# Kernel tuning notes

Measured on AMD Instinct MI355X. Metric: run time of the kernel, lower is better.

## Reference

```python
import jax, jax.numpy as jnp
import numpy as np


def setup_inputs() -> dict:
    key = jax.random.key(0)
    k1, k2, k3 = jax.random.split(key, 3)
    B, CIN, T, K = 64, 64, 1, 4096
    COUT, F = 64, 4
    L = F * K  # 16384; gather index space per (b, o)
    x = jax.random.normal(k1, (B, CIN, T, K), dtype=jnp.float32)
    upsample_params = jax.random.normal(k2, (CIN, COUT, F), dtype=jnp.float32)
    indices = jax.random.randint(k3, (L,), 0, L, dtype=jnp.int64 if jax.config.jax_enable_x64 else jnp.int32)
    return {"x": x, "upsample_params": upsample_params, "indices": indices}


def reference(x, upsample_params, indices):
    # x: [B, Cin, T, K]; params: [Cin, Cout, 4] -> res: [B, Cout, 4, K]
    res = jnp.einsum('bitk,iof->bofk', x, upsample_params)
    B, O = res.shape[0], res.shape[1]
    L = indices.shape[0]  # == 4*K
    # torch: flatten + index_select with per-(b,o) offset == gather along last axis
    flat = res.reshape(B, O, L)
    out = jnp.take(flat, indices, axis=2)
    return out.reshape(B, O, 1, L)
```

## Files before the change

kernel.cpp:

```cpp
#include <hip/hip_runtime.h>


typedef __attribute__((ext_vector_type(8))) short short8;
typedef __attribute__((ext_vector_type(4))) float floatx4;

#define NB    64
#define CIN   64
#define COUT  64
#define KDIM  4096
#define LDIM  16384
#define ITERS 8
#define BXS2  72
#define XT_BYTES ((size_t)NB * KDIM * CIN * 2)

__device__ __forceinline__ unsigned short f2bf(float f) {
  union { float f; unsigned u; } v; v.f = f;
  unsigned r = v.u + 0x7FFFu + ((v.u >> 16) & 1u);
  return (unsigned short)(r >> 16);
}

__global__ __launch_bounds__(256) void transpose_bf16(const float* __restrict__ x,
                                                      unsigned short* __restrict__ xt) {
  __shared__ float tile[64 * 65];
  const int t = threadIdx.x;
  const int b = blockIdx.y;
  const int k0 = blockIdx.x * 64;
  const float4* x4 = (const float4*)x;
#pragma unroll
  for (int p = 0; p < 4; ++p) {
    int i  = p * 16 + (t >> 4);
    int kq = t & 15;
    float4 v = x4[(size_t)(b * CIN + i) * (KDIM / 4) + (k0 >> 2) + kq];
    tile[i * 65 + kq * 4 + 0] = v.x;
    tile[i * 65 + kq * 4 + 1] = v.y;
    tile[i * 65 + kq * 4 + 2] = v.z;
    tile[i * 65 + kq * 4 + 3] = v.w;
  }
  __syncthreads();
  unsigned int* xt32 = (unsigned int*)xt;
  const int ip = (t & 31) * 2;
#pragma unroll
  for (int p = 0; p < 8; ++p) {
    int k = p * 8 + (t >> 5);
    unsigned lo = f2bf(tile[ip * 65 + k]);
    unsigned hi = f2bf(tile[(ip + 1) * 65 + k]);
    xt32[((size_t)b * KDIM + k0 + k) * (CIN / 2) + (ip >> 1)] = lo | (hi << 16);
  }
}

__global__ __launch_bounds__(256) void prepack_afrag(const float* __restrict__ p,
                                                     unsigned short* __restrict__ pb) {
  const int t = blockIdx.x * 256 + threadIdx.x;
  const int lane = t & 63;
  const int mk = t >> 6;
  const int mt = mk >> 3, kt = mk & 7;
  const int o = mt * 16 + (lane & 15);
  const int quad = lane >> 4;
#pragma unroll
  for (int j = 0; j < 8; ++j) {
    int s = kt * 32 + quad * 8 + j;
    int i = s & 63, g = s >> 6;
    pb[t * 8 + j] = f2bf(p[(i * COUT + o) * 4 + g]);
  }
}

__global__ __launch_bounds__(256, 4) void gemm_db(const unsigned short* __restrict__ xt,
                                                  const unsigned short* __restrict__ pb,
                                                  const int* __restrict__ idx,
                                                  float* __restrict__ out) {
  __shared__ __align__(16) unsigned short Bx[2][64 * BXS2];
  __shared__ int fpv[2][64];

  const int t = threadIdx.x;
  const int b = blockIdx.y;
  const int w = t >> 6;
  const int lane = t & 63;
  const int lane15 = lane & 15;
  const int quad = lane >> 4;

  short8 af[8];
  {
    const short8* pbv = (const short8*)pb;
#pragma unroll
    for (int kt = 0; kt < 8; ++kt)
      af[kt] = pbv[(w * 8 + kt) * 64 + lane];
  }

  const unsigned short* xb = xt + (size_t)b * KDIM * CIN;
  const int u = t & 3;
  const int lrow = t >> 2;
  const int lb0 = blockIdx.x * (ITERS * 64);

  uint4 d0, d1; int fp, ivn;
  {
    const int iv0 = idx[lb0 + lrow];
    const uint4* r0 = (const uint4*)(xb + (size_t)(iv0 & (KDIM - 1)) * CIN);
    d0 = r0[2 * u];
    d1 = r0[2 * u + 1];
    fp = iv0 >> 12;
    ivn = idx[lb0 + 64 + lrow];
  }

  const short8 z8 = {0, 0, 0, 0, 0, 0, 0, 0};

  for (int it = 0; it < ITERS; ++it) {
    const int p = it & 1;
    *(uint4*)&Bx[p][lrow * BXS2 + u * 16]     = d0;
    *(uint4*)&Bx[p][lrow * BXS2 + u * 16 + 8] = d1;
    if (u == 0) fpv[p][lrow] = fp;
    asm volatile("s_waitcnt lgkmcnt(0)" ::: "memory");
    __builtin_amdgcn_s_barrier();
    asm volatile("" ::: "memory");

    if (it + 1 < ITERS) {
      fp = ivn >> 12;
      const uint4* rn = (const uint4*)(xb + (size_t)(ivn & (KDIM - 1)) * CIN);
      d0 = rn[2 * u];
      d1 = rn[2 * u + 1];
      if (it + 2 < ITERS) ivn = idx[lb0 + (it + 2) * 64 + lrow];
    }

    floatx4 acc[4] = {floatx4{0.f, 0.f, 0.f, 0.f}, floatx4{0.f, 0.f, 0.f, 0.f},
                      floatx4{0.f, 0.f, 0.f, 0.f}, floatx4{0.f, 0.f, 0.f, 0.f}};
#pragma unroll
    for (int nt = 0; nt < 4; ++nt) {
      const int lr = nt * 16 + lane15;
      const short8 ev = *(const short8*)&Bx[p][lr * BXS2 + quad * 8];
      const short8 ov = *(const short8*)&Bx[p][lr * BXS2 + 32 + quad * 8];
      const int fpl = fpv[p][lr];
#pragma unroll
      for (int kt = 0; kt < 8; ++kt) {
        const short8 h  = (kt & 1) ? ov : ev;
        const short8 bf = (fpl == (kt >> 1)) ? h : z8;
        acc[nt] = __builtin_amdgcn_mfma_f32_16x16x32_bf16(af[kt], bf, acc[nt], 0, 0, 0);
      }
    }

    const int l_base = lb0 + it * 64;
#pragma unroll
    for (int nt = 0; nt < 4; ++nt) {
      const int l = l_base + nt * 16 + lane15;
#pragma unroll
      for (int r = 0; r < 4; ++r) {
        const int o = w * 16 + quad * 4 + r;
        __builtin_nontemporal_store(acc[nt][r], &out[((size_t)(b * COUT + o)) * LDIM + l]);
      }
    }
  }
}

extern "C" void kernel_launch(void* const* d_in, const int* in_sizes, int n_in,
                              void* d_out, int out_size, void* d_ws, size_t ws_size,
                              hipStream_t stream) {
  const float* x      = (const float*)d_in[0];
  const float* params = (const float*)d_in[1];
  const int*   idx    = (const int*)d_in[2];
  float* out = (float*)d_out;
  unsigned short* xt = (unsigned short*)d_ws;
  unsigned short* pb = (unsigned short*)((char*)d_ws + XT_BYTES);

  transpose_bf16<<<dim3(KDIM / 64, NB), 256, 0, stream>>>(x, xt);
  prepack_afrag<<<dim3(8), 256, 0, stream>>>(params, pb);
  gemm_db<<<dim3(LDIM / (64 * ITERS), NB), 256, 0, stream>>>(xt, pb, idx, out);
}
```

Baseline: 348.0 us.

## Halve per-block iterations, swizzle block-to-batch mapping, interleave MFMA chains

Each block now handles 4 iterations instead of 8, which doubles the grid. Block IDs are remapped so that each group of eight consecutive workgroups spans different batches, which spreads the L2/XCD footprint. The gather load now has each thread fetch one 16-byte chunk from two different rows instead of two chunks from one row, and the MFMA loop runs two independent accumulator chains together to hide MFMA latency. This adds more blocks and more A-fragment reloads per unit of work, with the risk of extra launch and prologue overhead.

```diff
diff --git a/kernel.cpp b/kernel.cpp
--- a/kernel.cpp
+++ b/kernel.cpp
@@ -9,7 +9,7 @@
 #define COUT  64
 #define KDIM  4096
 #define LDIM  16384
-#define ITERS 8
+#define ITERS 4
 #define BXS2  72
 #define XT_BYTES ((size_t)NB * KDIM * CIN * 2)
 
@@ -64,7 +64,7 @@
   }
 }
 
-__global__ __launch_bounds__(256, 4) void gemm_db(const unsigned short* __restrict__ xt,
+__global__ __launch_bounds__(256, 4) void gemm_v4(const unsigned short* __restrict__ xt,
                                                   const unsigned short* __restrict__ pb,
                                                   const int* __restrict__ idx,
                                                   float* __restrict__ out) {
@@ -72,7 +72,11 @@
   __shared__ int fpv[2][64];
 
   const int t = threadIdx.x;
-  const int b = blockIdx.y;
+  const int wg  = blockIdx.x + gridDim.x * blockIdx.y;
+  const int wgp = (wg & 7) * 512 + (wg >> 3);
+  const int b   = wgp >> 6;
+  const int xx  = wgp & 63;
+
   const int w = t >> 6;
   const int lane = t & 63;
   const int lane15 = lane & 15;
@@ -87,53 +91,64 @@
   }
 
   const unsigned short* xb = xt + (size_t)b * KDIM * CIN;
-  const int u = t & 3;
-  const int lrow = t >> 2;
-  const int lb0 = blockIdx.x * (ITERS * 64);
+  const int u  = t & 7;
+  const int r1 = t >> 3;
+  const int lb0 = xx * (ITERS * 64);
 
-  uint4 d0, d1; int fp, ivn;
-  {
-    const int iv0 = idx[lb0 + lrow];
-    const uint4* r0 = (const uint4*)(xb + (size_t)(iv0 & (KDIM - 1)) * CIN);
-    d0 = r0[2 * u];
-    d1 = r0[2 * u + 1];
-    fp = iv0 >> 12;
-    ivn = idx[lb0 + 64 + lrow];
-  }
+  int iv1 = idx[lb0 + r1];
+  int iv2 = idx[lb0 + 32 + r1];
+  uint4 d0 = ((const uint4*)(xb + (size_t)(iv1 & (KDIM - 1)) * CIN))[u];
+  uint4 d1 = ((const uint4*)(xb + (size_t)(iv2 & (KDIM - 1)) * CIN))[u];
+  int fp1 = iv1 >> 12, fp2 = iv2 >> 12;
+  int ivn1 = idx[lb0 + 64 + r1];
+  int ivn2 = idx[lb0 + 96 + r1];
 
   const short8 z8 = {0, 0, 0, 0, 0, 0, 0, 0};
 
   for (int it = 0; it < ITERS; ++it) {
     const int p = it & 1;
-    *(uint4*)&Bx[p][lrow * BXS2 + u * 16]     = d0;
-    *(uint4*)&Bx[p][lrow * BXS2 + u * 16 + 8] = d1;
-    if (u == 0) fpv[p][lrow] = fp;
+    *(uint4*)&Bx[p][r1 * BXS2 + u * 8]        = d0;
+    *(uint4*)&Bx[p][(r1 + 32) * BXS2 + u * 8] = d1;
+    if (u == 0) { fpv[p][r1] = fp1; fpv[p][r1 + 32] = fp2; }
     asm volatile("s_waitcnt lgkmcnt(0)" ::: "memory");
     __builtin_amdgcn_s_barrier();
     asm volatile("" ::: "memory");
 
     if (it + 1 < ITERS) {
-      fp = ivn >> 12;
-      const uint4* rn = (const uint4*)(xb + (size_t)(ivn & (KDIM - 1)) * CIN);
-      d0 = rn[2 * u];
-      d1 = rn[2 * u + 1];
-      if (it + 2 < ITERS) ivn = idx[lb0 + (it + 2) * 64 + lrow];
+      fp1 = ivn1 >> 12;
+      fp2 = ivn2 >> 12;
+      d0 = ((const uint4*)(xb + (size_t)(ivn1 & (KDIM - 1)) * CIN))[u];
+      d1 = ((const uint4*)(xb + (size_t)(ivn2 & (KDIM - 1)) * CIN))[u];
+      if (it + 2 < ITERS) {
+        ivn1 = idx[lb0 + (it + 2) * 64 + r1];
+        ivn2 = idx[lb0 + (it + 2) * 64 + 32 + r1];
+      }
     }
 
-    floatx4 acc[4] = {floatx4{0.f, 0.f, 0.f, 0.f}, floatx4{0.f, 0.f, 0.f, 0.f},
-                      floatx4{0.f, 0.f, 0.f, 0.f}, floatx4{0.f, 0.f, 0.f, 0.f}};
+    floatx4 acc[4];
 #pragma unroll
-    for (int nt = 0; nt < 4; ++nt) {
-      const int lr = nt * 16 + lane15;
-      const short8 ev = *(const short8*)&Bx[p][lr * BXS2 + quad * 8];
-      const short8 ov = *(const short8*)&Bx[p][lr * BXS2 + 32 + quad * 8];
-      const int fpl = fpv[p][lr];
+    for (int np = 0; np < 2; ++np) {
+      const int lrA = (np * 2) * 16 + lane15;
+      const int lrB = (np * 2 + 1) * 16 + lane15;
+      const short8 evA = *(const short8*)&Bx[p][lrA * BXS2 + quad * 8];
+      const short8 ovA = *(const short8*)&Bx[p][lrA * BXS2 + 32 + quad * 8];
+      const short8 evB = *(const short8*)&Bx[p][lrB * BXS2 + quad * 8];
+      const short8 ovB = *(const short8*)&Bx[p][lrB * BXS2 + 32 + quad * 8];
+      const int fA = fpv[p][lrA];
+      const int fB = fpv[p][lrB];
+      floatx4 a0 = floatx4{0.f, 0.f, 0.f, 0.f};
+      floatx4 a1 = floatx4{0.f, 0.f, 0.f, 0.f};
 #pragma unroll
       for (int kt = 0; kt < 8; ++kt) {
-        const short8 h  = (kt & 1) ? ov : ev;
-        const short8 bf = (fpl == (kt >> 1)) ? h : z8;
-        acc[nt] = __builtin_amdgcn_mfma_f32_16x16x32_bf16(af[kt], bf, acc[nt], 0, 0, 0);
+        const short8 hA = (kt & 1) ? ovA : evA;
+        const short8 hB = (kt & 1) ? ovB : evB;
+        const short8 bA = (fA == (kt >> 1)) ? hA : z8;
+        const short8 bB = (fB == (kt >> 1)) ? hB : z8;
+        a0 = __builtin_amdgcn_mfma_f32_16x16x32_bf16(af[kt], bA, a0, 0, 0, 0);
+        a1 = __builtin_amdgcn_mfma_f32_16x16x32_bf16(af[kt], bB, a1, 0, 0, 0);
       }
+      acc[np * 2]     = a0;
+      acc[np * 2 + 1] = a1;
     }
 
     const int l_base = lb0 + it * 64;
@@ -161,5 +176,5 @@
 
   transpose_bf16<<<dim3(KDIM / 64, NB), 256, 0, stream>>>(x, xt);
   prepack_afrag<<<dim3(8), 256, 0, stream>>>(params, pb);
-  gemm_db<<<dim3(LDIM / (64 * ITERS), NB), 256, 0, stream>>>(xt, pb, idx, out);
+  gemm_v4<<<dim3(LDIM / (64 * ITERS), NB), 256, 0, stream>>>(xt, pb, idx, out);
 }
```

Measured after the change: 347.8 us. About the same (-0.1%).
